# Kernel tuning notes

Hardware: AMD Instinct MI355X
Metric: run time of the kernel (lower is better)

The kernel has to match this reference:

```python
import jax, jax.numpy as jnp
import numpy as np

B, T, F = 512, 256, 128
H, FF, OUT = 512, 1024, 64
PAD = -999.0


def setup_inputs() -> dict:
    key = jax.random.key(0)
    ks = jax.random.split(key, 10)
    x = jax.random.normal(ks[0], (B, T, F), dtype=jnp.float32)
    seq_lens = jax.random.randint(ks[1], (B,), 0, T)
    seq_lens = jnp.maximum(seq_lens, 1)  # at least one valid timestep per sample
    # apply end-of-sequence padding with the padding indicator value
    t_idx = jnp.arange(T)
    pad_mask = t_idx[None, :] >= seq_lens[:, None]  # [B, T] True where padded
    x = jnp.where(pad_mask[:, :, None], PAD, x)
    s = 0.02
    W_ih = jax.random.normal(ks[2], (3 * H, F), dtype=jnp.float32) * s
    W_hh = jax.random.normal(ks[3], (3 * H, H), dtype=jnp.float32) * s
    b_ih = jax.random.normal(ks[4], (3 * H,), dtype=jnp.float32) * s
    b_hh = jax.random.normal(ks[5], (3 * H,), dtype=jnp.float32) * s
    W1 = jax.random.normal(ks[6], (H, FF), dtype=jnp.float32) * s
    b1 = jnp.zeros((FF,), dtype=jnp.float32)
    W2 = jax.random.normal(ks[7], (FF, OUT), dtype=jnp.float32) * s
    b2 = jnp.zeros((OUT,), dtype=jnp.float32)
    return {"x": x, "seq_lens": seq_lens, "W_ih": W_ih, "W_hh": W_hh,
            "b_ih": b_ih, "b_hh": b_hh, "W1": W1, "b1": b1, "W2": W2, "b2": b2}


def _run(x, seq_lens, W_ih, W_hh, b_ih, b_hh, W1, b1, W2, b2):
    valid = jnp.arange(T)[None, :] < seq_lens[:, None]  # [B, T]

    def gru_step(h, inp):
        x_t, v = inp  # x_t: [B, F], v: [B]
        gi = x_t @ W_ih.T + b_ih            # [B, 3H]
        gh = h @ W_hh.T + b_hh              # [B, 3H]
        i_r, i_z, i_n = jnp.split(gi, 3, axis=-1)
        h_r, h_z, h_n = jnp.split(gh, 3, axis=-1)
        r = jax.nn.sigmoid(i_r + h_r)
        z = jax.nn.sigmoid(i_z + h_z)
        n = jnp.tanh(i_n + r * h_n)
        h_new = (1.0 - z) * n + z * h
        # packed-sequence semantics: hidden only advances on valid steps;
        # padded output positions are filled with the padding indicator
        h = jnp.where(v[:, None], h_new, h)
        out = jnp.where(v[:, None], h_new, PAD)
        return h, out

    h0 = jnp.zeros((B, H), dtype=x.dtype)
    xs = (jnp.swapaxes(x, 0, 1), jnp.swapaxes(valid, 0, 1))  # time-major
    _, rnn_out_t = jax.lax.scan(gru_step, h0, xs)             # [T, B, H]
    rnn_out = jnp.swapaxes(rnn_out_t, 0, 1)                   # [B, T, H]

    # apply_to_each_timestep: FF head on non-padded rows only, padded rows
    # get fill value = padding_indicator
    ff_in = jnp.where(valid[:, :, None], rnn_out, 0.0)
    hid = jax.nn.relu(jnp.einsum('bth,hf->btf', ff_in, W1) + b1)
    y = jnp.einsum('btf,fo->bto', hid, W2) + b2               # [B, T, OUT]
    y = jnp.where(valid[:, :, None], y, PAD)
    return y


def reference(x, seq_lens, W_ih, W_hh, b_ih, b_hh, W1, b1, W2, b2):
    return _run(x, seq_lens, W_ih, W_hh, b_ih, b_hh, W1, b1, W2, b2)
```

## Files before the change

kernel.cpp:

```cpp
#include <hip/hip_runtime.h>

#define BB 512
#define TT 256
#define FDIM 128
#define HDIM 512
#define FFD 1024
#define OUTD 64
#define PADV -999.0f
#define NBLK 256
#define NTHR 256
#define PGRP (4 * 64 * 16)
#define PSLOT (8 * PGRP)

typedef __bf16 bf16_t;
typedef bf16_t bf16x8 __attribute__((ext_vector_type(8)));
typedef float f32x4 __attribute__((ext_vector_type(4)));
typedef unsigned int u32;
typedef u32 u32x4 __attribute__((ext_vector_type(4)));
typedef unsigned long long u64;

union LdsU {
  struct {
    u32 rzf[80 * 256];
    u32 nhf[32 * 256];
    u32 nif[8 * 256];
    float  ex[4][64][33];
    u64 hprev[64][8];
  } a;
  struct {
    u32 w1f[64 * 256];
    u32 w2f[8 * 256];
    bf16_t st[64 * 72];
  } b;
};

__device__ __forceinline__ f32x4 mfma16(bf16x8 a, bf16x8 b, f32x4 c) {
  return __builtin_amdgcn_mfma_f32_16x16x32_bf16(a, b, c, 0, 0, 0);
}
__device__ __forceinline__ float sigm(float x) { return 1.f / (1.f + __expf(-x)); }
__device__ __forceinline__ float tanh_f(float x) { return 2.f / (1.f + __expf(-2.f * x)) - 1.f; }

__device__ __forceinline__ void wait_flags(unsigned* f1, unsigned v1,
                                           unsigned* f2, unsigned v2) {
  const int l = threadIdx.x & 63;
  if (l < 32) {
    unsigned* p = (l < 16) ? (f1 + l) : (f2 + (l - 16));
    const unsigned v = (l < 16) ? v1 : v2;
    while (__hip_atomic_load(p, __ATOMIC_RELAXED, __HIP_MEMORY_SCOPE_AGENT) < v)
      __builtin_amdgcn_s_sleep(1);
  }
}


__global__ __launch_bounds__(NTHR) void gru_net_kernel(
    const float* __restrict__ x, const int* __restrict__ seq,
    const float* __restrict__ Wih, const float* __restrict__ Whh,
    const float* __restrict__ bih, const float* __restrict__ bhh,
    const float* __restrict__ W1, const float* __restrict__ b1,
    const float* __restrict__ W2, const float* __restrict__ b2,
    float* __restrict__ out,
    bf16_t* __restrict__ hb, bf16_t* __restrict__ ff, bf16_t* __restrict__ hd,
    float* __restrict__ psc, unsigned* __restrict__ bar) {
  __shared__ LdsU L;
  __shared__ float biasA[4][32];
  __shared__ float b1s[64];
  __shared__ float b2s[64];
  __shared__ int   seqA[64];
  __shared__ int   seqC[64];

  const int blk = blockIdx.x, tid = threadIdx.x;
  const int wv = tid >> 6, lane = tid & 63;
  const int q = lane >> 4, col16 = lane & 15, q8 = q * 8;
  const bool isA = blk < 128;

  const int grp = isA ? (blk & 7) : ((blk - 128) & 7);
  unsigned* flagA = bar + grp * 32;
  unsigned* flagB = bar + (8 + grp) * 32;

  int b0 = 0, c0 = 0, f0 = 0;
  if (isA) {
    const int sib = blk >> 3;
    b0 = (blk & 7) * 64;
    c0 = sib * 32;
    for (int i = tid; i < 80 * 64; i += NTHR) {
      const int ln = i & 63, fi = i >> 6;
      const int j = fi / 20, ks = fi - j * 20;
      const int cc = ln & 15, qq = ln >> 4;
      const int colj = j * 16 + cc;
      const int grow = (colj < 32) ? (c0 + colj) : (512 + c0 + (colj - 32));
      bf16_t tmp[8];
      if (ks < 4) {
        const float* src = Wih + (size_t)grow * FDIM + ks * 32 + qq * 8;
        for (int e = 0; e < 8; ++e) tmp[e] = (bf16_t)src[e];
      } else {
        const float* src = Whh + (size_t)grow * HDIM + (ks - 4) * 32 + qq * 8;
        for (int e = 0; e < 8; ++e) tmp[e] = (bf16_t)src[e];
      }
      const u32* t32 = (const u32*)tmp;
      u32* dst = &L.a.rzf[fi * 256 + ln];
      dst[0] = t32[0]; dst[64] = t32[1]; dst[128] = t32[2]; dst[192] = t32[3];
    }
    for (int i = tid; i < 32 * 64; i += NTHR) {
      const int ln = i & 63, fi = i >> 6;
      const int j2 = fi >> 4, ks = fi & 15;
      const int cc = ln & 15, qq = ln >> 4;
      const int grow = 1024 + c0 + j2 * 16 + cc;
      const float* src = Whh + (size_t)grow * HDIM + ks * 32 + qq * 8;
      bf16_t tmp[8];
      for (int e = 0; e < 8; ++e) tmp[e] = (bf16_t)src[e];
      const u32* t32 = (const u32*)tmp;
      u32* dst = &L.a.nhf[fi * 256 + ln];
      dst[0] = t32[0]; dst[64] = t32[1]; dst[128] = t32[2]; dst[192] = t32[3];
    }
    for (int i = tid; i < 8 * 64; i += NTHR) {
      const int ln = i & 63, fi = i >> 6;
      const int j2 = fi >> 2, ks = fi & 3;
      const int cc = ln & 15, qq = ln >> 4;
      const int grow = 1024 + c0 + j2 * 16 + cc;
      const float* src = Wih + (size_t)grow * FDIM + ks * 32 + qq * 8;
      bf16_t tmp[8];
      for (int e = 0; e < 8; ++e) tmp[e] = (bf16_t)src[e];
      const u32* t32 = (const u32*)tmp;
      u32* dst = &L.a.nif[fi * 256 + ln];
      dst[0] = t32[0]; dst[64] = t32[1]; dst[128] = t32[2]; dst[192] = t32[3];
    }
    if (tid < 32) {
      biasA[0][tid] = bih[c0 + tid] + bhh[c0 + tid];
      biasA[1][tid] = bih[512 + c0 + tid] + bhh[512 + c0 + tid];
      biasA[2][tid] = bih[1024 + c0 + tid];
      biasA[3][tid] = bhh[1024 + c0 + tid];
    }
    if (tid < 64) seqA[tid] = seq[b0 + tid];

    for (int i = tid; i < 512; i += NTHR) {
      const int r = i >> 3, cq = (i & 7) * 4;
      __hip_atomic_store((u64*)(hb + (size_t)BB * HDIM + (size_t)(b0 + r) * HDIM + c0 + cq),
                         0ull, __ATOMIC_RELAXED, __HIP_MEMORY_SCOPE_AGENT);
      ((u64*)L.a.hprev)[i] = 0ull;
    }
    __syncthreads();
    if (tid == 0)
      __hip_atomic_store(&flagA[sib], 1u, __ATOMIC_RELAXED, __HIP_MEMORY_SCOPE_AGENT);

    for (int t = 0; t < TT; ++t) {
      const int rA = b0 + wv * 16 + col16;
      const float* paxf = x + ((size_t)rA * TT + t) * FDIM;
      const f32x4 zz = {0.f, 0.f, 0.f, 0.f};
      f32x4 acc[4] = {zz, zz, zz, zz};
      f32x4 accn[2] = {zz, zz};
      f32x4 acci[2] = {zz, zz};
      #pragma unroll
      for (int ks = 0; ks < 4; ++ks) {
        const int ko = ks * 32 + q8;
        const float4 u0 = *(const float4*)(paxf + ko);
        const float4 u1 = *(const float4*)(paxf + ko + 4);
        bf16x8 av;
        av[0]=(bf16_t)u0.x; av[1]=(bf16_t)u0.y; av[2]=(bf16_t)u0.z; av[3]=(bf16_t)u0.w;
        av[4]=(bf16_t)u1.x; av[5]=(bf16_t)u1.y; av[6]=(bf16_t)u1.z; av[7]=(bf16_t)u1.w;
        #pragma unroll
        for (int j = 0; j < 4; ++j) {
          const u32* pz = &L.a.rzf[(size_t)(j * 20 + ks) * 256 + lane];
          const u32x4 tz = {pz[0], pz[64], pz[128], pz[192]};
          acc[j] = mfma16(av, *(const bf16x8*)&tz, acc[j]);
        }
        #pragma unroll
        for (int j = 0; j < 2; ++j) {
          const u32* pn = &L.a.nif[(size_t)(j * 4 + ks) * 256 + lane];
          const u32x4 tn = {pn[0], pn[64], pn[128], pn[192]};
          acci[j] = mfma16(av, *(const bf16x8*)&tn, acci[j]);
        }
      }
      if (wv == 0)
        wait_flags(flagA, (unsigned)(t + 1), flagB, (t >= 2) ? (unsigned)(t - 1) : 0u);
      __syncthreads();

      bf16_t* hr = hb + (size_t)((t + 1) & 1) * BB * HDIM;
      bf16_t* hw = hb + (size_t)(t & 1) * BB * HDIM;
      bf16_t* fw = ff + (size_t)(t & 1) * BB * HDIM;
      bf16_t* pah = hr + (size_t)rA * HDIM;
      #pragma unroll
      for (int kp = 0; kp < 4; ++kp) {
        const int ks0 = kp * 4, ks1 = kp * 4 + 1, ks2 = kp * 4 + 2, ks3 = kp * 4 + 3;
        const int ko0 = ks0 * 32 + q8, ko1 = ks1 * 32 + q8;
        const int ko2 = ks2 * 32 + q8, ko3 = ks3 * 32 + q8;
        u64 hqa[2];
        u64 hqb[2];
        u64 hqc[2];
        u64 hqd[2];
        hqa[0] = __hip_atomic_load((u64*)(pah + ko0),     __ATOMIC_RELAXED, __HIP_MEMORY_SCOPE_AGENT);
        hqa[1] = __hip_atomic_load((u64*)(pah + ko0) + 1, __ATOMIC_RELAXED, __HIP_MEMORY_SCOPE_AGENT);
        hqb[0] = __hip_atomic_load((u64*)(pah + ko1),     __ATOMIC_RELAXED, __HIP_MEMORY_SCOPE_AGENT);
        hqb[1] = __hip_atomic_load((u64*)(pah + ko1) + 1, __ATOMIC_RELAXED, __HIP_MEMORY_SCOPE_AGENT);
        hqc[0] = __hip_atomic_load((u64*)(pah + ko2),     __ATOMIC_RELAXED, __HIP_MEMORY_SCOPE_AGENT);
        hqc[1] = __hip_atomic_load((u64*)(pah + ko2) + 1, __ATOMIC_RELAXED, __HIP_MEMORY_SCOPE_AGENT);
        hqd[0] = __hip_atomic_load((u64*)(pah + ko3),     __ATOMIC_RELAXED, __HIP_MEMORY_SCOPE_AGENT);
        hqd[1] = __hip_atomic_load((u64*)(pah + ko3) + 1, __ATOMIC_RELAXED, __HIP_MEMORY_SCOPE_AGENT);
        const bf16x8 av0 = *(const bf16x8*)hqa;
        const bf16x8 av1 = *(const bf16x8*)hqb;
        const bf16x8 av2 = *(const bf16x8*)hqc;
        const bf16x8 av3 = *(const bf16x8*)hqd;
        #pragma unroll
        for (int j = 0; j < 4; ++j) {
          const u32* pz = &L.a.rzf[(size_t)(j * 20 + 4 + ks0) * 256 + lane];
          const u32x4 tz = {pz[0], pz[64], pz[128], pz[192]};
          acc[j] = mfma16(av0, *(const bf16x8*)&tz, acc[j]);
        }
        #pragma unroll
        for (int j = 0; j < 2; ++j) {
          const u32* pn = &L.a.nhf[(size_t)(j * 16 + ks0) * 256 + lane];
          const u32x4 tn = {pn[0], pn[64], pn[128], pn[192]};
          accn[j] = mfma16(av0, *(const bf16x8*)&tn, accn[j]);
        }
        #pragma unroll
        for (int j = 0; j < 4; ++j) {
          const u32* pz = &L.a.rzf[(size_t)(j * 20 + 4 + ks1) * 256 + lane];
          const u32x4 tz = {pz[0], pz[64], pz[128], pz[192]};
          acc[j] = mfma16(av1, *(const bf16x8*)&tz, acc[j]);
        }
        #pragma unroll
        for (int j = 0; j < 2; ++j) {
          const u32* pn = &L.a.nhf[(size_t)(j * 16 + ks1) * 256 + lane];
          const u32x4 tn = {pn[0], pn[64], pn[128], pn[192]};
          accn[j] = mfma16(av1, *(const bf16x8*)&tn, accn[j]);
        }
        #pragma unroll
        for (int j = 0; j < 4; ++j) {
          const u32* pz = &L.a.rzf[(size_t)(j * 20 + 4 + ks2) * 256 + lane];
          const u32x4 tz = {pz[0], pz[64], pz[128], pz[192]};
          acc[j] = mfma16(av2, *(const bf16x8*)&tz, acc[j]);
        }
        #pragma unroll
        for (int j = 0; j < 2; ++j) {
          const u32* pn = &L.a.nhf[(size_t)(j * 16 + ks2) * 256 + lane];
          const u32x4 tn = {pn[0], pn[64], pn[128], pn[192]};
          accn[j] = mfma16(av2, *(const bf16x8*)&tn, accn[j]);
        }
        #pragma unroll
        for (int j = 0; j < 4; ++j) {
          const u32* pz = &L.a.rzf[(size_t)(j * 20 + 4 + ks3) * 256 + lane];
          const u32x4 tz = {pz[0], pz[64], pz[128], pz[192]};
          acc[j] = mfma16(av3, *(const bf16x8*)&tz, acc[j]);
        }
        #pragma unroll
        for (int j = 0; j < 2; ++j) {
          const u32* pn = &L.a.nhf[(size_t)(j * 16 + ks3) * 256 + lane];
          const u32x4 tn = {pn[0], pn[64], pn[128], pn[192]};
          accn[j] = mfma16(av3, *(const bf16x8*)&tn, accn[j]);
        }
      }
      #pragma unroll
      for (int j = 0; j < 4; ++j) {
        const int sl = j >> 1, cb = (j & 1) * 16 + col16;
        #pragma unroll
        for (int rg = 0; rg < 4; ++rg)
          L.a.ex[sl][wv * 16 + q * 4 + rg][cb] = acc[j][rg];
      }
      #pragma unroll
      for (int j = 0; j < 2; ++j) {
        const int cb = j * 16 + col16;
        #pragma unroll
        for (int rg = 0; rg < 4; ++rg) {
          L.a.ex[2][wv * 16 + q * 4 + rg][cb] = accn[j][rg];
          L.a.ex[3][wv * 16 + q * 4 + rg][cb] = acci[j][rg];
        }
      }
      __syncthreads();
      for (int e = tid; e < 512; e += NTHR) {
        const int row = e >> 3, cq = (e & 7) << 2;
        const int bidx = b0 + row;
        const u64 hp8 = L.a.hprev[row][cq >> 2];
        const bf16_t* hp4 = (const bf16_t*)&hp8;
        bf16_t hw4[4], fw4[4];
        const bool v = (t < seqA[row]);
        #pragma unroll
        for (int j = 0; j < 4; ++j) {
          const int c = cq + j;
          const float gr  = L.a.ex[0][row][c] + biasA[0][c];
          const float gz  = L.a.ex[1][row][c] + biasA[1][c];
          const float gnh = L.a.ex[2][row][c] + biasA[3][c];
          const float gni = L.a.ex[3][row][c] + biasA[2][c];
          const float r = sigm(gr), zg = sigm(gz);
          const float n = tanh_f(gni + r * gnh);
          const float hp = (float)hp4[j];
          const float hnew = (1.f - zg) * n + zg * hp;
          hw4[j] = (bf16_t)(v ? hnew : hp);
          fw4[j] = (bf16_t)(v ? hnew : 0.f);
        }
        L.a.hprev[row][cq >> 2] = *(u64*)hw4;
        __hip_atomic_store((u64*)(hw + (size_t)bidx * HDIM + c0 + cq), *(u64*)hw4,
                           __ATOMIC_RELAXED, __HIP_MEMORY_SCOPE_AGENT);
        __hip_atomic_store((u64*)(fw + (size_t)bidx * HDIM + c0 + cq), *(u64*)fw4,
                           __ATOMIC_RELAXED, __HIP_MEMORY_SCOPE_AGENT);
      }
      __syncthreads();
      if (tid == 0)
        __hip_atomic_store(&flagA[sib], (unsigned)(t + 2), __ATOMIC_RELAXED, __HIP_MEMORY_SCOPE_AGENT);
    }
  } else {
    const int cidx = blk - 128;
    const int fc = cidx >> 3;
    const int oc = fc & 3;
    const int kq = fc >> 2;
    b0 = (cidx & 7) * 64;
    f0 = fc * 64;
    const int o0 = oc * 16;
    for (int i = tid; i < 64 * 64; i += NTHR) {
      const int ln = i & 63, fi = i >> 6;
      const int j = fi >> 4, ks = fi & 15;
      const int cc = ln & 15, qq = ln >> 4;
      const int fcol = f0 + j * 16 + cc;
      const int kb = ks * 32 + qq * 8;
      bf16_t tmp[8];
      for (int e = 0; e < 8; ++e) tmp[e] = (bf16_t)W1[(size_t)(kb + e) * FFD + fcol];
      const u32* t32 = (const u32*)tmp;
      u32* dst = &L.b.w1f[fi * 256 + ln];
      dst[0] = t32[0]; dst[64] = t32[1]; dst[128] = t32[2]; dst[192] = t32[3];
    }
    if (tid < 64) b1s[tid] = b1[f0 + tid];
    for (int i = tid; i < 8 * 64; i += NTHR) {
      const int ln = i & 63, ks = i >> 6;
      const int cc = ln & 15, qq = ln >> 4;
      const int kb = kq * 256 + ks * 32 + qq * 8;
      bf16_t tmp[8];
      for (int e = 0; e < 8; ++e) tmp[e] = (bf16_t)W2[(kb + e) * OUTD + o0 + cc];
      const u32* t32 = (const u32*)tmp;
      u32* dst = &L.b.w2f[ks * 256 + ln];
      dst[0] = t32[0]; dst[64] = t32[1]; dst[128] = t32[2]; dst[192] = t32[3];
    }
    if (tid < 64) b2s[tid] = b2[tid];
    if (tid < 64) seqC[tid] = seq[b0 + tid];
    __syncthreads();

    const int baseF = fc * 256 + tid;
    const int ocF = baseF >> 10, remF = baseF & 1023;
    const int rowF = remF >> 4, colF = remF & 15;

    float* pwB = psc + (size_t)kq * PSLOT + (size_t)grp * PGRP + (size_t)oc * (64 * 16);
    float* prB = psc + (size_t)grp * PGRP + (size_t)ocF * (64 * 16) + rowF * 16 + colF;

    for (int u = 0; u <= TT + 1; ++u) {
      if (wv == 0)
        wait_flags(flagB, (unsigned)u, flagA, (u < TT) ? (unsigned)(u + 2) : 0u);
      __syncthreads();

      const int rCF = b0 + wv * 16 + col16;
      bf16_t* paF = hd + (size_t)((u - 1) & 1) * BB * FFD + (size_t)rCF * FFD + kq * 256 + q8;
      u64 fz0a = 0, fz0b = 0, fz1a = 0, fz1b = 0, fz2a = 0, fz2b = 0, fz3a = 0, fz3b = 0;
      u64 fz4a = 0, fz4b = 0, fz5a = 0, fz5b = 0, fz6a = 0, fz6b = 0, fz7a = 0, fz7b = 0;
      if (u >= 1 && u <= TT) {
        fz0a = __hip_atomic_load((u64*)(paF + 0 * 32),     __ATOMIC_RELAXED, __HIP_MEMORY_SCOPE_AGENT);
        fz0b = __hip_atomic_load((u64*)(paF + 0 * 32) + 1, __ATOMIC_RELAXED, __HIP_MEMORY_SCOPE_AGENT);
        fz1a = __hip_atomic_load((u64*)(paF + 1 * 32),     __ATOMIC_RELAXED, __HIP_MEMORY_SCOPE_AGENT);
        fz1b = __hip_atomic_load((u64*)(paF + 1 * 32) + 1, __ATOMIC_RELAXED, __HIP_MEMORY_SCOPE_AGENT);
        fz2a = __hip_atomic_load((u64*)(paF + 2 * 32),     __ATOMIC_RELAXED, __HIP_MEMORY_SCOPE_AGENT);
        fz2b = __hip_atomic_load((u64*)(paF + 2 * 32) + 1, __ATOMIC_RELAXED, __HIP_MEMORY_SCOPE_AGENT);
        fz3a = __hip_atomic_load((u64*)(paF + 3 * 32),     __ATOMIC_RELAXED, __HIP_MEMORY_SCOPE_AGENT);
        fz3b = __hip_atomic_load((u64*)(paF + 3 * 32) + 1, __ATOMIC_RELAXED, __HIP_MEMORY_SCOPE_AGENT);
        fz4a = __hip_atomic_load((u64*)(paF + 4 * 32),     __ATOMIC_RELAXED, __HIP_MEMORY_SCOPE_AGENT);
        fz4b = __hip_atomic_load((u64*)(paF + 4 * 32) + 1, __ATOMIC_RELAXED, __HIP_MEMORY_SCOPE_AGENT);
        fz5a = __hip_atomic_load((u64*)(paF + 5 * 32),     __ATOMIC_RELAXED, __HIP_MEMORY_SCOPE_AGENT);
        fz5b = __hip_atomic_load((u64*)(paF + 5 * 32) + 1, __ATOMIC_RELAXED, __HIP_MEMORY_SCOPE_AGENT);
        fz6a = __hip_atomic_load((u64*)(paF + 6 * 32),     __ATOMIC_RELAXED, __HIP_MEMORY_SCOPE_AGENT);
        fz6b = __hip_atomic_load((u64*)(paF + 6 * 32) + 1, __ATOMIC_RELAXED, __HIP_MEMORY_SCOPE_AGENT);
        fz7a = __hip_atomic_load((u64*)(paF + 7 * 32),     __ATOMIC_RELAXED, __HIP_MEMORY_SCOPE_AGENT);
        fz7b = __hip_atomic_load((u64*)(paF + 7 * 32) + 1, __ATOMIC_RELAXED, __HIP_MEMORY_SCOPE_AGENT);
      }
      float* ppF = prB + (size_t)((u - 2) & 1) * (4 * PSLOT);
      u32 fp0 = 0, fp1 = 0, fp2 = 0, fp3 = 0;
      if (u >= 2) {
        fp0 = __hip_atomic_load((u32*)(ppF + 0 * PSLOT), __ATOMIC_RELAXED, __HIP_MEMORY_SCOPE_AGENT);
        fp1 = __hip_atomic_load((u32*)(ppF + 1 * PSLOT), __ATOMIC_RELAXED, __HIP_MEMORY_SCOPE_AGENT);
        fp2 = __hip_atomic_load((u32*)(ppF + 2 * PSLOT), __ATOMIC_RELAXED, __HIP_MEMORY_SCOPE_AGENT);
        fp3 = __hip_atomic_load((u32*)(ppF + 3 * PSLOT), __ATOMIC_RELAXED, __HIP_MEMORY_SCOPE_AGENT);
      }

      if (u < TT) {
        const int t = u;
        bf16_t* fr = ff + (size_t)(t & 1) * BB * HDIM;
        bf16_t* hwid = hd + (size_t)(t & 1) * BB * FFD;
        const int rB = b0 + wv * 16 + col16;
        bf16_t* pa = fr + (size_t)rB * HDIM;
        const f32x4 zz = {0.f, 0.f, 0.f, 0.f};
        f32x4 acc[4] = {zz, zz, zz, zz};
        #pragma unroll
        for (int kp = 0; kp < 4; ++kp) {
          const int ks0 = kp * 4, ks1 = kp * 4 + 1, ks2 = kp * 4 + 2, ks3 = kp * 4 + 3;
          const int ko0 = ks0 * 32 + q8, ko1 = ks1 * 32 + q8;
          const int ko2 = ks2 * 32 + q8, ko3 = ks3 * 32 + q8;
          u64 fqa[2];
          u64 fqb[2];
          u64 fqc[2];
          u64 fqd[2];
          fqa[0] = __hip_atomic_load((u64*)(pa + ko0),     __ATOMIC_RELAXED, __HIP_MEMORY_SCOPE_AGENT);
          fqa[1] = __hip_atomic_load((u64*)(pa + ko0) + 1, __ATOMIC_RELAXED, __HIP_MEMORY_SCOPE_AGENT);
          fqb[0] = __hip_atomic_load((u64*)(pa + ko1),     __ATOMIC_RELAXED, __HIP_MEMORY_SCOPE_AGENT);
          fqb[1] = __hip_atomic_load((u64*)(pa + ko1) + 1, __ATOMIC_RELAXED, __HIP_MEMORY_SCOPE_AGENT);
          fqc[0] = __hip_atomic_load((u64*)(pa + ko2),     __ATOMIC_RELAXED, __HIP_MEMORY_SCOPE_AGENT);
          fqc[1] = __hip_atomic_load((u64*)(pa + ko2) + 1, __ATOMIC_RELAXED, __HIP_MEMORY_SCOPE_AGENT);
          fqd[0] = __hip_atomic_load((u64*)(pa + ko3),     __ATOMIC_RELAXED, __HIP_MEMORY_SCOPE_AGENT);
          fqd[1] = __hip_atomic_load((u64*)(pa + ko3) + 1, __ATOMIC_RELAXED, __HIP_MEMORY_SCOPE_AGENT);
          const bf16x8 av0 = *(const bf16x8*)fqa;
          const bf16x8 av1 = *(const bf16x8*)fqb;
          const bf16x8 av2 = *(const bf16x8*)fqc;
          const bf16x8 av3 = *(const bf16x8*)fqd;
          #pragma unroll
          for (int j = 0; j < 4; ++j) {
            const u32* pw = &L.b.w1f[(size_t)(j * 16 + ks0) * 256 + lane];
            const u32x4 tw = {pw[0], pw[64], pw[128], pw[192]};
            acc[j] = mfma16(av0, *(const bf16x8*)&tw, acc[j]);
          }
          #pragma unroll
          for (int j = 0; j < 4; ++j) {
            const u32* pw = &L.b.w1f[(size_t)(j * 16 + ks1) * 256 + lane];
            const u32x4 tw = {pw[0], pw[64], pw[128], pw[192]};
            acc[j] = mfma16(av1, *(const bf16x8*)&tw, acc[j]);
          }
          #pragma unroll
          for (int j = 0; j < 4; ++j) {
            const u32* pw = &L.b.w1f[(size_t)(j * 16 + ks2) * 256 + lane];
            const u32x4 tw = {pw[0], pw[64], pw[128], pw[192]};
            acc[j] = mfma16(av2, *(const bf16x8*)&tw, acc[j]);
          }
          #pragma unroll
          for (int j = 0; j < 4; ++j) {
            const u32* pw = &L.b.w1f[(size_t)(j * 16 + ks3) * 256 + lane];
            const u32x4 tw = {pw[0], pw[64], pw[128], pw[192]};
            acc[j] = mfma16(av3, *(const bf16x8*)&tw, acc[j]);
          }
        }
        #pragma unroll
        for (int j = 0; j < 4; ++j) {
          const int fcc = j * 16 + col16;
          #pragma unroll
          for (int rg = 0; rg < 4; ++rg)
            L.b.st[(wv * 16 + q * 4 + rg) * 72 + fcc] =
                (bf16_t)fmaxf(acc[j][rg] + b1s[fcc], 0.f);
        }
        __syncthreads();
        for (int w = tid; w < 1024; w += NTHR) {
          const int r = w >> 4, cq = (w & 15) * 4;
          const u64 pk = *(const u64*)&L.b.st[r * 72 + cq];
          __hip_atomic_store((u64*)(hwid + (size_t)(b0 + r) * FFD + f0 + cq), pk,
                             __ATOMIC_RELAXED, __HIP_MEMORY_SCOPE_AGENT);
        }
      }
      if (u >= 1 && u <= TT) {
        const int t = u - 1;
        f32x4 acc = {0.f, 0.f, 0.f, 0.f};
        {
          u64 w0[2] = {fz0a, fz0b};
          const u32* pw = &L.b.w2f[(size_t)0 * 256 + lane];
          const u32x4 tw = {pw[0], pw[64], pw[128], pw[192]};
          acc = mfma16(*(const bf16x8*)w0, *(const bf16x8*)&tw, acc);
        }
        {
          u64 w1v[2] = {fz1a, fz1b};
          const u32* pw = &L.b.w2f[(size_t)1 * 256 + lane];
          const u32x4 tw = {pw[0], pw[64], pw[128], pw[192]};
          acc = mfma16(*(const bf16x8*)w1v, *(const bf16x8*)&tw, acc);
        }
        {
          u64 w2v[2] = {fz2a, fz2b};
          const u32* pw = &L.b.w2f[(size_t)2 * 256 + lane];
          const u32x4 tw = {pw[0], pw[64], pw[128], pw[192]};
          acc = mfma16(*(const bf16x8*)w2v, *(const bf16x8*)&tw, acc);
        }
        {
          u64 w3v[2] = {fz3a, fz3b};
          const u32* pw = &L.b.w2f[(size_t)3 * 256 + lane];
          const u32x4 tw = {pw[0], pw[64], pw[128], pw[192]};
          acc = mfma16(*(const bf16x8*)w3v, *(const bf16x8*)&tw, acc);
        }
        {
          u64 w4v[2] = {fz4a, fz4b};
          const u32* pw = &L.b.w2f[(size_t)4 * 256 + lane];
          const u32x4 tw = {pw[0], pw[64], pw[128], pw[192]};
          acc = mfma16(*(const bf16x8*)w4v, *(const bf16x8*)&tw, acc);
        }
        {
          u64 w5v[2] = {fz5a, fz5b};
          const u32* pw = &L.b.w2f[(size_t)5 * 256 + lane];
          const u32x4 tw = {pw[0], pw[64], pw[128], pw[192]};
          acc = mfma16(*(const bf16x8*)w5v, *(const bf16x8*)&tw, acc);
        }
        {
          u64 w6v[2] = {fz6a, fz6b};
          const u32* pw = &L.b.w2f[(size_t)6 * 256 + lane];
          const u32x4 tw = {pw[0], pw[64], pw[128], pw[192]};
          acc = mfma16(*(const bf16x8*)w6v, *(const bf16x8*)&tw, acc);
        }
        {
          u64 w7v[2] = {fz7a, fz7b};
          const u32* pw = &L.b.w2f[(size_t)7 * 256 + lane];
          const u32x4 tw = {pw[0], pw[64], pw[128], pw[192]};
          acc = mfma16(*(const bf16x8*)w7v, *(const bf16x8*)&tw, acc);
        }
        float* pb = pwB + (size_t)(t & 1) * (4 * PSLOT);
        #pragma unroll
        for (int rg = 0; rg < 4; ++rg) {
          float vv = acc[rg];
          __hip_atomic_store((u32*)(pb + (wv * 16 + q * 4 + rg) * 16 + col16),
                             *(u32*)&vv, __ATOMIC_RELAXED, __HIP_MEMORY_SCOPE_AGENT);
        }
      }
      if (u >= 2) {
        const int t2 = u - 2;
        float p0, p1, p2, p3;
        *(u32*)&p0 = fp0; *(u32*)&p1 = fp1; *(u32*)&p2 = fp2; *(u32*)&p3 = fp3;
        const float pv = (p0 + p1) + (p2 + p3);
        const bool v = (t2 < seqC[rowF]);
        out[((size_t)(b0 + rowF) * TT + t2) * OUTD + ocF * 16 + colF] =
            v ? (pv + b2s[ocF * 16 + colF]) : PADV;
      }
      __syncthreads();
      if (tid == 0)
        __hip_atomic_store(&flagB[fc], (unsigned)(u + 1), __ATOMIC_RELAXED, __HIP_MEMORY_SCOPE_AGENT);
    }
  }
}

extern "C" void kernel_launch(void* const* d_in, const int* in_sizes, int n_in,
                              void* d_out, int out_size, void* d_ws, size_t ws_size,
                              hipStream_t stream) {
  const float* x   = (const float*)d_in[0];
  const int*   seq = (const int*)d_in[1];
  const float* Wih = (const float*)d_in[2];
  const float* Whh = (const float*)d_in[3];
  const float* bih = (const float*)d_in[4];
  const float* bhh = (const float*)d_in[5];
  const float* W1  = (const float*)d_in[6];
  const float* b1  = (const float*)d_in[7];
  const float* W2  = (const float*)d_in[8];
  const float* b2  = (const float*)d_in[9];
  float* out = (float*)d_out;
  char* ws = (char*)d_ws;

  unsigned* bar = (unsigned*)ws;
  float* psc = (float*)(ws + 4096);
  bf16_t* hb = (bf16_t*)(ws + 4096 + (size_t)2 * 4 * PSLOT * 4);
  bf16_t* ff = hb + (size_t)2 * BB * HDIM;
  bf16_t* hd = ff + (size_t)2 * BB * HDIM;

  hipMemsetAsync(ws, 0, 4096, stream);
  void* args[] = {&x, &seq, &Wih, &Whh, &bih, &bhh, &W1, &b1, &W2, &b2,
                  &out, &hb, &ff, &hd, &psc, &bar};
  hipLaunchCooperativeKernel((void*)gru_net_kernel, dim3(NBLK), dim3(NTHR),
                             args, 0, stream);
}
```

Before: 2.098 ms.

## Fuse second FF matmul into first-stage blocks with split-K partial sums

Each FF block now multiplies its 64-column hidden slice, still in LDS, by the matching 64-row slice of W2 right after computing the ReLU. It writes 64x64 partial outputs per feature chunk to global scratch, and the reduction at the next step sums 16 partials instead of 4. This removes the round trip of the full bf16 hidden activations through global memory, and with it one pipeline stage, so the loop runs TT+1 iterations. The cost is more partial-sum traffic: 16 atomic loads per output element, and each block writes a 64x64 tile instead of 64x16.

```diff
diff --git a/kernel.cpp b/kernel.cpp
--- a/kernel.cpp
+++ b/kernel.cpp
@@ -9,8 +9,8 @@
 #define PADV -999.0f
 #define NBLK 256
 #define NTHR 256
-#define PGRP (4 * 64 * 16)
-#define PSLOT (8 * PGRP)
+#define PTILE 4096
+#define PPLANE (8 * PTILE)
 
 typedef __bf16 bf16_t;
 typedef bf16_t bf16x8 __attribute__((ext_vector_type(8)));
@@ -59,7 +59,7 @@
     const float* __restrict__ W1, const float* __restrict__ b1,
     const float* __restrict__ W2, const float* __restrict__ b2,
     float* __restrict__ out,
-    bf16_t* __restrict__ hb, bf16_t* __restrict__ ff, bf16_t* __restrict__ hd,
+    bf16_t* __restrict__ hb, bf16_t* __restrict__ ff,
     float* __restrict__ psc, unsigned* __restrict__ bar) {
   __shared__ LdsU L;
   __shared__ float biasA[4][32];
@@ -299,11 +299,8 @@
   } else {
     const int cidx = blk - 128;
     const int fc = cidx >> 3;
-    const int oc = fc & 3;
-    const int kq = fc >> 2;
     b0 = (cidx & 7) * 64;
     f0 = fc * 64;
-    const int o0 = oc * 16;
     for (int i = tid; i < 64 * 64; i += NTHR) {
       const int ln = i & 63, fi = i >> 6;
       const int j = fi >> 4, ks = fi & 15;
@@ -318,13 +315,14 @@
     }
     if (tid < 64) b1s[tid] = b1[f0 + tid];
     for (int i = tid; i < 8 * 64; i += NTHR) {
-      const int ln = i & 63, ks = i >> 6;
+      const int ln = i & 63, fi = i >> 6;
+      const int j = fi >> 1, ks = fi & 1;
       const int cc = ln & 15, qq = ln >> 4;
-      const int kb = kq * 256 + ks * 32 + qq * 8;
+      const int kb = f0 + ks * 32 + qq * 8;
       bf16_t tmp[8];
-      for (int e = 0; e < 8; ++e) tmp[e] = (bf16_t)W2[(kb + e) * OUTD + o0 + cc];
+      for (int e = 0; e < 8; ++e) tmp[e] = (bf16_t)W2[(size_t)(kb + e) * OUTD + j * 16 + cc];
       const u32* t32 = (const u32*)tmp;
-      u32* dst = &L.b.w2f[ks * 256 + ln];
+      u32* dst = &L.b.w2f[fi * 256 + ln];
       dst[0] = t32[0]; dst[64] = t32[1]; dst[128] = t32[2]; dst[192] = t32[3];
     }
     if (tid < 64) b2s[tid] = b2[tid];
@@ -332,52 +330,41 @@
     __syncthreads();
 
     const int baseF = fc * 256 + tid;
-    const int ocF = baseF >> 10, remF = baseF & 1023;
-    const int rowF = remF >> 4, colF = remF & 15;
-
-    float* pwB = psc + (size_t)kq * PSLOT + (size_t)grp * PGRP + (size_t)oc * (64 * 16);
-    float* prB = psc + (size_t)grp * PGRP + (size_t)ocF * (64 * 16) + rowF * 16 + colF;
-
-    for (int u = 0; u <= TT + 1; ++u) {
+    const int rowF = baseF >> 6, colF = baseF & 63;
+
+    float* pwB = psc + ((size_t)fc * 8 + grp) * PTILE;
+    float* prB = psc + (size_t)grp * PTILE + rowF * 64 + colF;
+
+    for (int u = 0; u <= TT; ++u) {
       if (wv == 0)
         wait_flags(flagB, (unsigned)u, flagA, (u < TT) ? (unsigned)(u + 2) : 0u);
       __syncthreads();
 
-      const int rCF = b0 + wv * 16 + col16;
-      bf16_t* paF = hd + (size_t)((u - 1) & 1) * BB * FFD + (size_t)rCF * FFD + kq * 256 + q8;
-      u64 fz0a = 0, fz0b = 0, fz1a = 0, fz1b = 0, fz2a = 0, fz2b = 0, fz3a = 0, fz3b = 0;
-      u64 fz4a = 0, fz4b = 0, fz5a = 0, fz5b = 0, fz6a = 0, fz6b = 0, fz7a = 0, fz7b = 0;
-      if (u >= 1 && u <= TT) {
-        fz0a = __hip_atomic_load((u64*)(paF + 0 * 32),     __ATOMIC_RELAXED, __HIP_MEMORY_SCOPE_AGENT);
-        fz0b = __hip_atomic_load((u64*)(paF + 0 * 32) + 1, __ATOMIC_RELAXED, __HIP_MEMORY_SCOPE_AGENT);
-        fz1a = __hip_atomic_load((u64*)(paF + 1 * 32),     __ATOMIC_RELAXED, __HIP_MEMORY_SCOPE_AGENT);
-        fz1b = __hip_atomic_load((u64*)(paF + 1 * 32) + 1, __ATOMIC_RELAXED, __HIP_MEMORY_SCOPE_AGENT);
-        fz2a = __hip_atomic_load((u64*)(paF + 2 * 32),     __ATOMIC_RELAXED, __HIP_MEMORY_SCOPE_AGENT);
-        fz2b = __hip_atomic_load((u64*)(paF + 2 * 32) + 1, __ATOMIC_RELAXED, __HIP_MEMORY_SCOPE_AGENT);
-        fz3a = __hip_atomic_load((u64*)(paF + 3 * 32),     __ATOMIC_RELAXED, __HIP_MEMORY_SCOPE_AGENT);
-        fz3b = __hip_atomic_load((u64*)(paF + 3 * 32) + 1, __ATOMIC_RELAXED, __HIP_MEMORY_SCOPE_AGENT);
-        fz4a = __hip_atomic_load((u64*)(paF + 4 * 32),     __ATOMIC_RELAXED, __HIP_MEMORY_SCOPE_AGENT);
-        fz4b = __hip_atomic_load((u64*)(paF + 4 * 32) + 1, __ATOMIC_RELAXED, __HIP_MEMORY_SCOPE_AGENT);
-        fz5a = __hip_atomic_load((u64*)(paF + 5 * 32),     __ATOMIC_RELAXED, __HIP_MEMORY_SCOPE_AGENT);
-        fz5b = __hip_atomic_load((u64*)(paF + 5 * 32) + 1, __ATOMIC_RELAXED, __HIP_MEMORY_SCOPE_AGENT);
-        fz6a = __hip_atomic_load((u64*)(paF + 6 * 32),     __ATOMIC_RELAXED, __HIP_MEMORY_SCOPE_AGENT);
-        fz6b = __hip_atomic_load((u64*)(paF + 6 * 32) + 1, __ATOMIC_RELAXED, __HIP_MEMORY_SCOPE_AGENT);
-        fz7a = __hip_atomic_load((u64*)(paF + 7 * 32),     __ATOMIC_RELAXED, __HIP_MEMORY_SCOPE_AGENT);
-        fz7b = __hip_atomic_load((u64*)(paF + 7 * 32) + 1, __ATOMIC_RELAXED, __HIP_MEMORY_SCOPE_AGENT);
-      }
-      float* ppF = prB + (size_t)((u - 2) & 1) * (4 * PSLOT);
-      u32 fp0 = 0, fp1 = 0, fp2 = 0, fp3 = 0;
-      if (u >= 2) {
-        fp0 = __hip_atomic_load((u32*)(ppF + 0 * PSLOT), __ATOMIC_RELAXED, __HIP_MEMORY_SCOPE_AGENT);
-        fp1 = __hip_atomic_load((u32*)(ppF + 1 * PSLOT), __ATOMIC_RELAXED, __HIP_MEMORY_SCOPE_AGENT);
-        fp2 = __hip_atomic_load((u32*)(ppF + 2 * PSLOT), __ATOMIC_RELAXED, __HIP_MEMORY_SCOPE_AGENT);
-        fp3 = __hip_atomic_load((u32*)(ppF + 3 * PSLOT), __ATOMIC_RELAXED, __HIP_MEMORY_SCOPE_AGENT);
+      float* pr = prB + (size_t)((u - 1) & 1) * (16 * PPLANE);
+      u32 fp0 = 0, fp1 = 0, fp2 = 0, fp3 = 0, fp4 = 0, fp5 = 0, fp6 = 0, fp7 = 0;
+      u32 fp8 = 0, fp9 = 0, fp10 = 0, fp11 = 0, fp12 = 0, fp13 = 0, fp14 = 0, fp15 = 0;
+      if (u >= 1) {
+        fp0  = __hip_atomic_load((u32*)(pr + 0  * PPLANE), __ATOMIC_RELAXED, __HIP_MEMORY_SCOPE_AGENT);
+        fp1  = __hip_atomic_load((u32*)(pr + 1  * PPLANE), __ATOMIC_RELAXED, __HIP_MEMORY_SCOPE_AGENT);
+        fp2  = __hip_atomic_load((u32*)(pr + 2  * PPLANE), __ATOMIC_RELAXED, __HIP_MEMORY_SCOPE_AGENT);
+        fp3  = __hip_atomic_load((u32*)(pr + 3  * PPLANE), __ATOMIC_RELAXED, __HIP_MEMORY_SCOPE_AGENT);
+        fp4  = __hip_atomic_load((u32*)(pr + 4  * PPLANE), __ATOMIC_RELAXED, __HIP_MEMORY_SCOPE_AGENT);
+        fp5  = __hip_atomic_load((u32*)(pr + 5  * PPLANE), __ATOMIC_RELAXED, __HIP_MEMORY_SCOPE_AGENT);
+        fp6  = __hip_atomic_load((u32*)(pr + 6  * PPLANE), __ATOMIC_RELAXED, __HIP_MEMORY_SCOPE_AGENT);
+        fp7  = __hip_atomic_load((u32*)(pr + 7  * PPLANE), __ATOMIC_RELAXED, __HIP_MEMORY_SCOPE_AGENT);
+        fp8  = __hip_atomic_load((u32*)(pr + 8  * PPLANE), __ATOMIC_RELAXED, __HIP_MEMORY_SCOPE_AGENT);
+        fp9  = __hip_atomic_load((u32*)(pr + 9  * PPLANE), __ATOMIC_RELAXED, __HIP_MEMORY_SCOPE_AGENT);
+        fp10 = __hip_atomic_load((u32*)(pr + 10 * PPLANE), __ATOMIC_RELAXED, __HIP_MEMORY_SCOPE_AGENT);
+        fp11 = __hip_atomic_load((u32*)(pr + 11 * PPLANE), __ATOMIC_RELAXED, __HIP_MEMORY_SCOPE_AGENT);
+        fp12 = __hip_atomic_load((u32*)(pr + 12 * PPLANE), __ATOMIC_RELAXED, __HIP_MEMORY_SCOPE_AGENT);
+        fp13 = __hip_atomic_load((u32*)(pr + 13 * PPLANE), __ATOMIC_RELAXED, __HIP_MEMORY_SCOPE_AGENT);
+        fp14 = __hip_atomic_load((u32*)(pr + 14 * PPLANE), __ATOMIC_RELAXED, __HIP_MEMORY_SCOPE_AGENT);
+        fp15 = __hip_atomic_load((u32*)(pr + 15 * PPLANE), __ATOMIC_RELAXED, __HIP_MEMORY_SCOPE_AGENT);
       }
 
       if (u < TT) {
         const int t = u;
         bf16_t* fr = ff + (size_t)(t & 1) * BB * HDIM;
-        bf16_t* hwid = hd + (size_t)(t & 1) * BB * FFD;
         const int rB = b0 + wv * 16 + col16;
         bf16_t* pa = fr + (size_t)rB * HDIM;
         const f32x4 zz = {0.f, 0.f, 0.f, 0.f};
@@ -437,80 +424,55 @@
                 (bf16_t)fmaxf(acc[j][rg] + b1s[fcc], 0.f);
         }
         __syncthreads();
-        for (int w = tid; w < 1024; w += NTHR) {
-          const int r = w >> 4, cq = (w & 15) * 4;
-          const u64 pk = *(const u64*)&L.b.st[r * 72 + cq];
-          __hip_atomic_store((u64*)(hwid + (size_t)(b0 + r) * FFD + f0 + cq), pk,
-                             __ATOMIC_RELAXED, __HIP_MEMORY_SCOPE_AGENT);
-        }
-      }
-      if (u >= 1 && u <= TT) {
-        const int t = u - 1;
-        f32x4 acc = {0.f, 0.f, 0.f, 0.f};
+        f32x4 a2[4] = {zz, zz, zz, zz};
         {
-          u64 w0[2] = {fz0a, fz0b};
-          const u32* pw = &L.b.w2f[(size_t)0 * 256 + lane];
-          const u32x4 tw = {pw[0], pw[64], pw[128], pw[192]};
-          acc = mfma16(*(const bf16x8*)w0, *(const bf16x8*)&tw, acc);
+          const bf16x8 av = *(const bf16x8*)&L.b.st[(wv * 16 + col16) * 72 + 0 * 32 + q8];
+          #pragma unroll
+          for (int j = 0; j < 4; ++j) {
+            const u32* pw = &L.b.w2f[(size_t)(j * 2 + 0) * 256 + lane];
+            const u32x4 tw = {pw[0], pw[64], pw[128], pw[192]};
+            a2[j] = mfma16(av, *(const bf16x8*)&tw, a2[j]);
+          }
         }
         {
-          u64 w1v[2] = {fz1a, fz1b};
-          const u32* pw = &L.b.w2f[(size_t)1 * 256 + lane];
-          const u32x4 tw = {pw[0], pw[64], pw[128], pw[192]};
-          acc = mfma16(*(const bf16x8*)w1v, *(const bf16x8*)&tw, acc);
-        }
+          const bf16x8 av = *(const bf16x8*)&L.b.st[(wv * 16 + col16) * 72 + 1 * 32 + q8];
+          #pragma unroll
+          for (int j = 0; j < 4; ++j) {
+            const u32* pw = &L.b.w2f[(size_t)(j * 2 + 1) * 256 + lane];
+            const u32x4 tw = {pw[0], pw[64], pw[128], pw[192]};
+            a2[j] = mfma16(av, *(const bf16x8*)&tw, a2[j]);
+          }
+        }
+        float* pb = pwB + (size_t)(u & 1) * (16 * PPLANE);
+        #pragma unroll
+        for (int j = 0; j < 4; ++j) {
+          #pragma unroll
+          for (int rg = 0; rg < 4; ++rg) {
+            float vv = a2[j][rg];
+            __hip_atomic_store((u32*)(pb + (wv * 16 + q * 4 + rg) * 64 + j * 16 + col16),
+                               *(u32*)&vv, __ATOMIC_RELAXED, __HIP_MEMORY_SCOPE_AGENT);
+          }
+        }
+      }
+      if (u >= 1) {
+        const int t2 = u - 1;
+        float p[4];
         {
-          u64 w2v[2] = {fz2a, fz2b};
-          const u32* pw = &L.b.w2f[(size_t)2 * 256 + lane];
-          const u32x4 tw = {pw[0], pw[64], pw[128], pw[192]};
-          acc = mfma16(*(const bf16x8*)w2v, *(const bf16x8*)&tw, acc);
-        }
-        {
-          u64 w3v[2] = {fz3a, fz3b};
-          const u32* pw = &L.b.w2f[(size_t)3 * 256 + lane];
-          const u32x4 tw = {pw[0], pw[64], pw[128], pw[192]};
-          acc = mfma16(*(const bf16x8*)w3v, *(const bf16x8*)&tw, acc);
-        }
-        {
-          u64 w4v[2] = {fz4a, fz4b};
-          const u32* pw = &L.b.w2f[(size_t)4 * 256 + lane];
-          const u32x4 tw = {pw[0], pw[64], pw[128], pw[192]};
-          acc = mfma16(*(const bf16x8*)w4v, *(const bf16x8*)&tw, acc);
-        }
-        {
-          u64 w5v[2] = {fz5a, fz5b};
-          const u32* pw = &L.b.w2f[(size_t)5 * 256 + lane];
-          const u32x4 tw = {pw[0], pw[64], pw[128], pw[192]};
-          acc = mfma16(*(const bf16x8*)w5v, *(const bf16x8*)&tw, acc);
-        }
-        {
-          u64 w6v[2] = {fz6a, fz6b};
-          const u32* pw = &L.b.w2f[(size_t)6 * 256 + lane];
-          const u32x4 tw = {pw[0], pw[64], pw[128], pw[192]};
-          acc = mfma16(*(const bf16x8*)w6v, *(const bf16x8*)&tw, acc);
-        }
-        {
-          u64 w7v[2] = {fz7a, fz7b};
-          const u32* pw = &L.b.w2f[(size_t)7 * 256 + lane];
-          const u32x4 tw = {pw[0], pw[64], pw[128], pw[192]};
-          acc = mfma16(*(const bf16x8*)w7v, *(const bf16x8*)&tw, acc);
-        }
-        float* pb = pwB + (size_t)(t & 1) * (4 * PSLOT);
-        #pragma unroll
-        for (int rg = 0; rg < 4; ++rg) {
-          float vv = acc[rg];
-          __hip_atomic_store((u32*)(pb + (wv * 16 + q * 4 + rg) * 16 + col16),
-                             *(u32*)&vv, __ATOMIC_RELAXED, __HIP_MEMORY_SCOPE_AGENT);
-        }
-      }
-      if (u >= 2) {
-        const int t2 = u - 2;
-        float p0, p1, p2, p3;
-        *(u32*)&p0 = fp0; *(u32*)&p1 = fp1; *(u32*)&p2 = fp2; *(u32*)&p3 = fp3;
-        const float pv = (p0 + p1) + (p2 + p3);
+          float a0, a1, a2v, a3, a4, a5, a6, a7;
+          float a8, a9, a10, a11, a12, a13, a14, a15;
+          *(u32*)&a0 = fp0;   *(u32*)&a1 = fp1;   *(u32*)&a2v = fp2;  *(u32*)&a3 = fp3;
+          *(u32*)&a4 = fp4;   *(u32*)&a5 = fp5;   *(u32*)&a6 = fp6;   *(u32*)&a7 = fp7;
+          *(u32*)&a8 = fp8;   *(u32*)&a9 = fp9;   *(u32*)&a10 = fp10; *(u32*)&a11 = fp11;
+          *(u32*)&a12 = fp12; *(u32*)&a13 = fp13; *(u32*)&a14 = fp14; *(u32*)&a15 = fp15;
+          p[0] = (a0 + a1) + (a2v + a3);
+          p[1] = (a4 + a5) + (a6 + a7);
+          p[2] = (a8 + a9) + (a10 + a11);
+          p[3] = (a12 + a13) + (a14 + a15);
+        }
+        const float pv = (p[0] + p[1]) + (p[2] + p[3]);
         const bool v = (t2 < seqC[rowF]);
-        out[((size_t)(b0 + rowF) * TT + t2) * OUTD + ocF * 16 + colF] =
-            v ? (pv + b2s[ocF * 16 + colF]) : PADV;
+        out[((size_t)(b0 + rowF) * TT + t2) * OUTD + colF] =
+            v ? (pv + b2s[colF]) : PADV;
       }
       __syncthreads();
       if (tid == 0)
@@ -537,13 +499,12 @@
 
   unsigned* bar = (unsigned*)ws;
   float* psc = (float*)(ws + 4096);
-  bf16_t* hb = (bf16_t*)(ws + 4096 + (size_t)2 * 4 * PSLOT * 4);
+  bf16_t* hb = (bf16_t*)(ws + 4096 + (size_t)2 * 16 * 8 * 4096 * 4);
   bf16_t* ff = hb + (size_t)2 * BB * HDIM;
-  bf16_t* hd = ff + (size_t)2 * BB * HDIM;
 
   hipMemsetAsync(ws, 0, 4096, stream);
   void* args[] = {&x, &seq, &Wih, &Whh, &bih, &bhh, &W1, &b1, &W2, &b2,
-                  &out, &hb, &ff, &hd, &psc, &bar};
+                  &out, &hb, &ff, &psc, &bar};
   hipLaunchCooperativeKernel((void*)gru_net_kernel, dim3(NBLK), dim3(NTHR),
                              args, 0, stream);
 }
```

Measured after the change: 2.141 ms. 1.02x slower.
